# Kernel tuning notes

Hardware: AMD Instinct MI355X
Metric: run time of the kernel (lower is better)

## Reference

```python
import jax, jax.numpy as jnp
import numpy as np

N_NODES = 20000
N_EDGES = 640000
D_IN = 128
D_OUT = 128


def _weighted_mean_aggr(x, src, dst, ew, n):
    # mean over incoming edges of (edge_weight * x_src) -> [n, d]
    msg = x[src] * ew[:, None]                          # [E, d]
    s = jax.ops.segment_sum(msg, dst, num_segments=n)   # [n, d]
    cnt = jax.ops.segment_sum(jnp.ones_like(ew), dst, num_segments=n)
    return s / jnp.maximum(cnt, 1.0)[:, None]


def setup_inputs() -> dict:
    key = jax.random.key(0)
    ks = jax.random.split(key, 12)
    scale_x = 1.0 / np.sqrt(D_IN)
    scale_h = 1.0 / np.sqrt(D_OUT)
    return {
        "X": jax.random.normal(ks[0], (N_NODES, D_IN), jnp.float32),
        "edge_index": jax.random.randint(ks[1], (2, N_EDGES), 0, N_NODES),
        "edge_weight": jax.random.uniform(ks[2], (N_EDGES,), jnp.float32),
        "H": jax.random.normal(ks[3], (N_NODES, D_OUT), jnp.float32),
        "C": jax.random.normal(ks[4], (N_NODES, D_OUT), jnp.float32),
        # stacked gate weights, gate order: [i, f, c, o]
        "Wx_l": jax.random.normal(ks[5], (4, D_IN, D_OUT), jnp.float32) * scale_x,
        "Wx_r": jax.random.normal(ks[6], (4, D_IN, D_OUT), jnp.float32) * scale_x,
        "bx": jnp.zeros((4, D_OUT), jnp.float32),
        "Wh_l": jax.random.normal(ks[7], (4, D_OUT, D_OUT), jnp.float32) * scale_h,
        "Wh_r": jax.random.normal(ks[8], (4, D_OUT, D_OUT), jnp.float32) * scale_h,
        "bh": jnp.zeros((4, D_OUT), jnp.float32),
        # peephole weights, order [i, f, o]
        "wc": jax.random.normal(ks[9], (3, D_OUT), jnp.float32) * scale_h,
        "bg": jnp.zeros((4, D_OUT), jnp.float32),
    }


def reference(X, edge_index, edge_weight, H, C, Wx_l, Wx_r, bx, Wh_l, Wh_r, bh, wc, bg):
    n = X.shape[0]
    src, dst = edge_index[0], edge_index[1]

    # Shared weighted-mean aggregations (identical graph for all 8 convs)
    aggX = _weighted_mean_aggr(X, src, dst, edge_weight, n)   # [N, D_IN]
    aggH = _weighted_mean_aggr(H, src, dst, edge_weight, n)   # [N, D_OUT]

    # WeightedSAGEConv per gate: lin_l(aggr) + lin_r(x) + bias; stacked over 4 gates
    Gx = jnp.einsum('nd,gdo->gno', aggX, Wx_l) + jnp.einsum('nd,gdo->gno', X, Wx_r) + bx[:, None, :]
    Gh = jnp.einsum('nd,gdo->gno', aggH, Wh_l) + jnp.einsum('nd,gdo->gno', H, Wh_r) + bh[:, None, :]
    G = Gx + Gh                                               # [4, N, D_OUT], order i,f,c,o

    I = jax.nn.sigmoid(G[0] + wc[0] * C + bg[0])
    F = jax.nn.sigmoid(G[1] + wc[1] * C + bg[1])
    T = jnp.tanh(G[2] + bg[2])
    C_new = F * C + I * T
    O = jax.nn.sigmoid(G[3] + wc[2] * C_new + bg[3])
    H_new = O * jnp.tanh(C_new)
    return (H_new, C_new)
```

## Files before the change

### kernel.cpp

```cpp
#include <hip/hip_runtime.h>
#include <math.h>

#define NN 20000
#define NE 640000
#define D  128
#define NSLICE 2500
#define NTILES 625
#define SEG 128

typedef __attribute__((ext_vector_type(8))) short short8;
typedef __attribute__((ext_vector_type(4))) float floatx4;

static __device__ __forceinline__ unsigned short f2bf(float f) {
    union { float f; unsigned int u; } v; v.f = f;
    unsigned int u = v.u;
    u += 0x7fff + ((u >> 16) & 1);
    return (unsigned short)(u >> 16);
}
static __device__ __forceinline__ unsigned int pack2bf(float a, float b) {
    return (unsigned int)f2bf(a) | ((unsigned int)f2bf(b) << 16);
}
static __device__ __forceinline__ float bf_lo(unsigned int u) {
    union { unsigned int i; float f; } v; v.i = u << 16; return v.f;
}
static __device__ __forceinline__ float bf_hi(unsigned int u) {
    union { unsigned int i; float f; } v; v.i = u & 0xffff0000u; return v.f;
}
static __device__ __forceinline__ float sigm(float x) { return 1.f / (1.f + __expf(-x)); }
static __device__ __forceinline__ float tanhx(float x) { return 1.f - 2.f / (__expf(2.f * x) + 1.f); }

static __device__ __forceinline__ void load_lds16(const void* g, void* l) {
    __builtin_amdgcn_global_load_lds(
        (const __attribute__((address_space(1))) unsigned int*)g,
        (__attribute__((address_space(3))) unsigned int*)l, 16, 0, 0);
}

__global__ void __launch_bounds__(256)
prep_fill_kernel(const int* __restrict__ src, const int* __restrict__ dst,
                 const float* __restrict__ ew, int* __restrict__ cnt,
                 unsigned int* __restrict__ s_p,
                 const float4* __restrict__ X4, const float4* __restrict__ H4,
                 unsigned int* __restrict__ XH32,
                 const float* __restrict__ Wx_l, const float* __restrict__ Wx_r,
                 const float* __restrict__ Wh_l, const float* __restrict__ Wh_r,
                 const float* __restrict__ bx, const float* __restrict__ bh,
                 const float* __restrict__ bg,
                 unsigned short* __restrict__ Wsz, float* __restrict__ bias) {
    int tid = threadIdx.x, b = blockIdx.x;
    for (int t = b * 256 + tid; t < NE; t += 640 * 256) {
        float4 x = X4[t];
        float4 h = H4[t];
        int n = t >> 5, q = t & 31;
        unsigned int* row = XH32 + n * 128;
        row[2 * q]          = pack2bf(x.x, x.y);
        row[2 * q + 1]      = pack2bf(x.z, x.w);
        row[64 + 2 * q]     = pack2bf(h.x, h.y);
        row[64 + 2 * q + 1] = pack2bf(h.z, h.w);
        if (t < 512 * 512) {
            int j = t >> 9, k = t & 511, g = j >> 7, o = j & 127;
            float w;
            if (k < 128)      w = Wx_l[g * 16384 + k * 128 + o];
            else if (k < 256) w = Wx_r[g * 16384 + (k - 128) * 128 + o];
            else if (k < 384) w = Wh_l[g * 16384 + (k - 256) * 128 + o];
            else              w = Wh_r[g * 16384 + (k - 384) * 128 + o];
            int ci = k >> 5, jg = (k >> 3) & 3, off = k & 7;
            Wsz[ci * 16384 + jg * 4096 + j * 8 + off] = f2bf(w);
            if (k == 0) bias[j] = bx[g * 128 + o] + bh[g * 128 + o] + bg[g * 128 + o];
        }
    }
    int s = b & 7, chunk = b >> 3;
    int lo = s * NSLICE, hi = lo + NSLICE;
    int e0 = chunk * 8000;
    for (int e = e0 + tid; e < e0 + 8000; e += 256) {
        int d = dst[e];
        if (d >= lo && d < hi) {
            int p = atomicAdd(&cnt[d], 1);
            if (p < SEG) s_p[d * SEG + p] = (unsigned int)src[e] | ((unsigned int)f2bf(ew[e]) << 16);
        }
    }
}

__global__ void __launch_bounds__(256)
aggregate_kernel(const uint2* __restrict__ XH64,
                 const int* __restrict__ cnt,
                 const unsigned int* __restrict__ s_p,
                 uint2* __restrict__ AGG64) {
    int wv = threadIdx.x >> 6, lane = threadIdx.x & 63;
    int b = blockIdx.x;
    int s = b & 7, j = b >> 3;
    int n = s * NSLICE + j * 4 + wv;
    int deg = cnt[n];
    int m = (deg < SEG) ? deg : SEG;
    const unsigned int* seg = s_p + (size_t)n * SEG;
    float a0 = 0.f, a1 = 0.f, a2 = 0.f, a3 = 0.f;
    int i = 0;
    for (; i + 16 <= m; i += 16) {
        unsigned int e[16];
        uint2 u[16];
#pragma unroll
        for (int k = 0; k < 16; ++k) e[k] = seg[i + k];
#pragma unroll
        for (int k = 0; k < 16; ++k) u[k] = XH64[(size_t)(e[k] & 0xffff) * 64 + lane];
#pragma unroll
        for (int k = 0; k < 16; ++k) {
            float w = __int_as_float(e[k] & 0xffff0000u);
            a0 += bf_lo(u[k].x) * w;
            a1 += bf_hi(u[k].x) * w;
            a2 += bf_lo(u[k].y) * w;
            a3 += bf_hi(u[k].y) * w;
        }
    }
    for (; i + 4 <= m; i += 4) {
        unsigned int e[4];
        uint2 u[4];
#pragma unroll
        for (int k = 0; k < 4; ++k) e[k] = seg[i + k];
#pragma unroll
        for (int k = 0; k < 4; ++k) u[k] = XH64[(size_t)(e[k] & 0xffff) * 64 + lane];
#pragma unroll
        for (int k = 0; k < 4; ++k) {
            float w = __int_as_float(e[k] & 0xffff0000u);
            a0 += bf_lo(u[k].x) * w;
            a1 += bf_hi(u[k].x) * w;
            a2 += bf_lo(u[k].y) * w;
            a3 += bf_hi(u[k].y) * w;
        }
    }
    for (; i < m; ++i) {
        unsigned int e = seg[i];
        float w = __int_as_float(e & 0xffff0000u);
        uint2 u = XH64[(size_t)(e & 0xffff) * 64 + lane];
        a0 += bf_lo(u.x) * w;
        a1 += bf_hi(u.x) * w;
        a2 += bf_lo(u.y) * w;
        a3 += bf_hi(u.y) * w;
    }
    float inv = (deg > 0) ? 1.0f / (float)deg : 1.0f;
    uint2 r;
    r.x = pack2bf(a0 * inv, a1 * inv);
    r.y = pack2bf(a2 * inv, a3 * inv);
    AGG64[(size_t)n * 64 + lane] = r;
}

__global__ void __launch_bounds__(256)
gemm_lstm_kernel(const unsigned short* __restrict__ XH,
                 const unsigned short* __restrict__ AGG,
                 const unsigned short* __restrict__ Wsz,
                 const float* __restrict__ bias,
                 const float* __restrict__ wc,
                 const float* __restrict__ C,
                 float* __restrict__ out) {
    __shared__ __align__(16) short Bs[2][8192];

    int tid = threadIdx.x;
    int wv = tid >> 6, lane = tid & 63;
    int lm = lane & 15, lq = lane >> 4;
    int bid = blockIdx.x;
    int m0 = (bid >> 1) * 32;
    int hb = (bid & 1) * 512;

    floatx4 acc[2][4];
#pragma unroll
    for (int mt = 0; mt < 2; ++mt)
#pragma unroll
        for (int g = 0; g < 4; ++g) acc[mt][g] = (floatx4)(0.f);

#pragma unroll
    for (int g = 0; g < 4; ++g)
        load_lds16(Wsz + wv * 4096 + g * 1024 + hb + lane * 8,
                   &Bs[0][wv * 2048 + g * 512]);

    short8 ca0, ca1;
    {
        const unsigned short* ar = AGG + (size_t)(m0 + lm) * 256 + lq * 8;
        ca0 = *(const short8*)ar;
        ca1 = *(const short8*)(ar + 16 * 256);
    }

    for (int it = 0; it < 16; ++it) {
        __syncthreads();
        if (it < 15) {
            const unsigned short* wb = Wsz + (it + 1) * 16384 + wv * 4096 + hb;
            short* lb = &Bs[(it + 1) & 1][wv * 2048];
#pragma unroll
            for (int g = 0; g < 4; ++g)
                load_lds16(wb + g * 1024 + lane * 8, &lb[g * 512]);
        }
        short8 na0, na1;
        if (it < 15) {
            int kn = (it + 1) * 32;
            const unsigned short* ab = (kn & 128) ? XH : AGG;
            int aoff = (kn & 127) | ((kn & 256) >> 1);
            const unsigned short* arn = ab + (size_t)(m0 + lm) * 256 + aoff + lq * 8;
            na0 = *(const short8*)arn;
            na1 = *(const short8*)(arn + 16 * 256);
        }
        const short* bsc = Bs[it & 1];
#pragma unroll
        for (int g = 0; g < 4; ++g) {
            short8 bfr = *(const short8*)&bsc[(lq << 11) + (g << 9) + ((wv << 4) + lm) * 8];
            acc[0][g] = __builtin_amdgcn_mfma_f32_16x16x32_bf16(ca0, bfr, acc[0][g], 0, 0, 0);
            acc[1][g] = __builtin_amdgcn_mfma_f32_16x16x32_bf16(ca1, bfr, acc[1][g], 0, 0, 0);
        }
        ca0 = na0; ca1 = na1;
    }

    int cg0 = (hb >> 3) + (wv << 4) + lm;
    float bG[4], wP[3];
#pragma unroll
    for (int g = 0; g < 4; ++g) bG[g] = bias[(g << 7) + cg0];
#pragma unroll
    for (int j = 0; j < 3; ++j) wP[j] = wc[j * 128 + cg0];

#pragma unroll
    for (int mt = 0; mt < 2; ++mt)
#pragma unroll
        for (int r = 0; r < 4; ++r) {
            int row = m0 + mt * 16 + lq * 4 + r;
            float c = C[(size_t)row * D + cg0];
            float pi = acc[mt][0][r] + bG[0] + wP[0] * c;
            float pf = acc[mt][1][r] + bG[1] + wP[1] * c;
            float pt = acc[mt][2][r] + bG[2];
            float po = acc[mt][3][r] + bG[3];
            float I = sigm(pi);
            float F = sigm(pf);
            float T = tanhx(pt);
            float cn = F * c + I * T;
            float O = sigm(po + wP[2] * cn);
            out[(size_t)row * D + cg0] = O * tanhx(cn);
            out[(size_t)NN * D + (size_t)row * D + cg0] = cn;
        }
}

extern "C" void kernel_launch(void* const* d_in, const int* in_sizes, int n_in,
                              void* d_out, int out_size, void* d_ws, size_t ws_size,
                              hipStream_t stream) {
    const float* X  = (const float*)d_in[0];
    const int* ei   = (const int*)d_in[1];
    const float* ew = (const float*)d_in[2];
    const float* H  = (const float*)d_in[3];
    const float* C  = (const float*)d_in[4];
    const float* Wx_l = (const float*)d_in[5];
    const float* Wx_r = (const float*)d_in[6];
    const float* bx   = (const float*)d_in[7];
    const float* Wh_l = (const float*)d_in[8];
    const float* Wh_r = (const float*)d_in[9];
    const float* bh   = (const float*)d_in[10];
    const float* wc   = (const float*)d_in[11];
    const float* bg   = (const float*)d_in[12];
    float* out = (float*)d_out;

    const int* src = ei;
    const int* dst = ei + NE;

    char* ws = (char*)d_ws;
    int* cnt = (int*)(ws + 0);
    unsigned int* s_p = (unsigned int*)(ws + 80128);
    unsigned short* XH  = (unsigned short*)(ws + 10320128);
    unsigned short* AGG = (unsigned short*)(ws + 20560128);
    unsigned short* Wsz = (unsigned short*)(ws + 30800128);
    float* bias = (float*)(ws + 31324416);

    hipMemsetAsync(cnt, 0, NN * sizeof(int), stream);
    prep_fill_kernel<<<640, 256, 0, stream>>>(src, dst, ew, cnt, s_p,
                                              (const float4*)X, (const float4*)H,
                                              (unsigned int*)XH,
                                              Wx_l, Wx_r, Wh_l, Wh_r,
                                              bx, bh, bg, Wsz, bias);
    aggregate_kernel<<<NN / 4, 256, 0, stream>>>((const uint2*)XH, cnt, s_p,
                                                 (uint2*)AGG);
    gemm_lstm_kernel<<<NTILES * 2, 256, 0, stream>>>(XH, AGG, Wsz, bias, wc, C, out);
}
```

Baseline: 224.7 us.

## Spread prep work over more blocks with vectorized edge and weight loads

The prep kernel now launches 5120 blocks instead of 640, with one element per thread rather than grid-stride loops. Dedicated block ranges handle bf16 packing of X and H and the weight swizzle. The weight swizzle now reads float4 rows coalesced instead of strided scalars. Edge data is loaded as int4/float4 before the conversion work so the latency overlaps, and each of 250 threads handles 4 edges in 1000-edge chunks. The goal is more parallelism and latency hiding in the memory-bound prep phase, at the cost of every block rereading edges filtered by slice and more atomics spread across blocks.

```diff
diff --git a/kernel.cpp b/kernel.cpp
--- a/kernel.cpp
+++ b/kernel.cpp
@@ -7,6 +7,8 @@
 #define NSLICE 2500
 #define NTILES 625
 #define SEG 128
+#define NCHUNK 640
+#define CHUNK 1000
 
 typedef __attribute__((ext_vector_type(8))) short short8;
 typedef __attribute__((ext_vector_type(4))) float floatx4;
@@ -47,35 +49,67 @@
                  const float* __restrict__ bg,
                  unsigned short* __restrict__ Wsz, float* __restrict__ bias) {
     int tid = threadIdx.x, b = blockIdx.x;
-    for (int t = b * 256 + tid; t < NE; t += 640 * 256) {
-        float4 x = X4[t];
-        float4 h = H4[t];
-        int n = t >> 5, q = t & 31;
-        unsigned int* row = XH32 + n * 128;
-        row[2 * q]          = pack2bf(x.x, x.y);
-        row[2 * q + 1]      = pack2bf(x.z, x.w);
-        row[64 + 2 * q]     = pack2bf(h.x, h.y);
-        row[64 + 2 * q + 1] = pack2bf(h.z, h.w);
-        if (t < 512 * 512) {
-            int j = t >> 9, k = t & 511, g = j >> 7, o = j & 127;
-            float w;
-            if (k < 128)      w = Wx_l[g * 16384 + k * 128 + o];
-            else if (k < 256) w = Wx_r[g * 16384 + (k - 128) * 128 + o];
-            else if (k < 384) w = Wh_l[g * 16384 + (k - 256) * 128 + o];
-            else              w = Wh_r[g * 16384 + (k - 384) * 128 + o];
-            int ci = k >> 5, jg = (k >> 3) & 3, off = k & 7;
-            Wsz[ci * 16384 + jg * 4096 + j * 8 + off] = f2bf(w);
-            if (k == 0) bias[j] = bx[g * 128 + o] + bh[g * 128 + o] + bg[g * 128 + o];
-        }
-    }
-    int s = b & 7, chunk = b >> 3;
+
+    int chunk = b >> 3, s = b & 7;
     int lo = s * NSLICE, hi = lo + NSLICE;
-    int e0 = chunk * 8000;
-    for (int e = e0 + tid; e < e0 + 8000; e += 256) {
-        int d = dst[e];
-        if (d >= lo && d < hi) {
-            int p = atomicAdd(&cnt[d], 1);
-            if (p < SEG) s_p[d * SEG + p] = (unsigned int)src[e] | ((unsigned int)f2bf(ew[e]) << 16);
+    int4 d4, sr4; float4 w4;
+    bool fill = (tid < 250);
+    if (fill) {
+        int e0 = chunk * CHUNK + tid * 4;
+        d4  = *(const int4*)(dst + e0);
+        sr4 = *(const int4*)(src + e0);
+        w4  = *(const float4*)(ew + e0);
+    }
+
+    if (b < 2560) {
+        int t = b * 256 + tid;
+        if (t < NE) {
+            float4 x = X4[t];
+            float4 h = H4[t];
+            int n = t >> 5, q = t & 31;
+            unsigned int* row = XH32 + n * 128;
+            row[2 * q]          = pack2bf(x.x, x.y);
+            row[2 * q + 1]      = pack2bf(x.z, x.w);
+            row[64 + 2 * q]     = pack2bf(h.x, h.y);
+            row[64 + 2 * q + 1] = pack2bf(h.z, h.w);
+        }
+    } else if (b < 2816) {
+        int t = (b - 2560) * 256 + tid;
+        int row = t >> 5;
+        int g = row >> 9, k = row & 511;
+        int o = (t & 31) * 4;
+        const float* Wb; int kk;
+        if (k < 128)      { Wb = Wx_l; kk = k; }
+        else if (k < 256) { Wb = Wx_r; kk = k - 128; }
+        else if (k < 384) { Wb = Wh_l; kk = k - 256; }
+        else              { Wb = Wh_r; kk = k - 384; }
+        float4 w = *(const float4*)(Wb + g * 16384 + kk * 128 + o);
+        int ci = k >> 5, jg = (k >> 3) & 3, off = k & 7;
+        unsigned short* wp = Wsz + ci * 16384 + jg * 4096 + (g * 128 + o) * 8 + off;
+        wp[0]  = f2bf(w.x);
+        wp[8]  = f2bf(w.y);
+        wp[16] = f2bf(w.z);
+        wp[24] = f2bf(w.w);
+        if (k == 0) {
+            int j0 = g * 128 + o;
+#pragma unroll
+            for (int i = 0; i < 4; ++i)
+                bias[j0 + i] = bx[j0 + i] + bh[j0 + i] + bg[j0 + i];
+        }
+    }
+
+    if (fill) {
+        int dv[4] = {d4.x, d4.y, d4.z, d4.w};
+        int sv[4] = {sr4.x, sr4.y, sr4.z, sr4.w};
+        float wv[4] = {w4.x, w4.y, w4.z, w4.w};
+#pragma unroll
+        for (int k = 0; k < 4; ++k) {
+            int d = dv[k];
+            if (d >= lo && d < hi) {
+                int p = atomicAdd(&cnt[d], 1);
+                if (p < SEG)
+                    s_p[d * SEG + p] = (unsigned int)sv[k] | ((unsigned int)f2bf(wv[k]) << 16);
+            }
         }
     }
 }
@@ -262,11 +296,11 @@
     float* bias = (float*)(ws + 31324416);
 
     hipMemsetAsync(cnt, 0, NN * sizeof(int), stream);
-    prep_fill_kernel<<<640, 256, 0, stream>>>(src, dst, ew, cnt, s_p,
-                                              (const float4*)X, (const float4*)H,
-                                              (unsigned int*)XH,
-                                              Wx_l, Wx_r, Wh_l, Wh_r,
-                                              bx, bh, bg, Wsz, bias);
+    prep_fill_kernel<<<5120, 256, 0, stream>>>(src, dst, ew, cnt, s_p,
+                                               (const float4*)X, (const float4*)H,
+                                               (unsigned int*)XH,
+                                               Wx_l, Wx_r, Wh_l, Wh_r,
+                                               bx, bh, bg, Wsz, bias);
     aggregate_kernel<<<NN / 4, 256, 0, stream>>>((const uint2*)XH, cnt, s_p,
                                                  (uint2*)AGG);
     gemm_lstm_kernel<<<NTILES * 2, 256, 0, stream>>>(XH, AGG, Wsz, bias, wc, C, out);
```

Result: faster. 207.3 us (-7.7%).
